# Kernel optimization log

Measured on AMD Instinct MI355X. Metric: run time of the kernel, lower is better.

Reference implementation:

```python
import jax, jax.numpy as jnp
import numpy as np

B, L, D, H = 2, 2048, 2048, 16
HD = D // H          # head_dim = 128
LAT = HD // 4        # latent_dim = 32


def setup_inputs() -> dict:
    key = jax.random.key(0)
    ks = jax.random.split(key, 16)
    def w(k, shape, fan_in):
        return jax.random.normal(k, shape, jnp.float32) / np.float32(np.sqrt(fan_in))
    x = jax.random.normal(ks[0], (B, L, D), jnp.float32)
    # RoPE frequencies, stored as (cos, sin) pairs: [L, HD//2, 2]
    inv_freq = 1.0 / (10000.0 ** (np.arange(0, HD, 2, dtype=np.float32) / HD))
    ang = np.outer(np.arange(L, dtype=np.float32), inv_freq)
    freqs_cis = jnp.stack([jnp.asarray(np.cos(ang)), jnp.asarray(np.sin(ang))], axis=-1)
    return dict(
        x=x, freqs_cis=freqs_cis,
        Wq=w(ks[1], (D, D), D), bq=jnp.zeros((D,), jnp.float32),
        Wk=w(ks[2], (D, D), D), bk=jnp.zeros((D,), jnp.float32),
        Wv=w(ks[3], (D, D), D), bv=jnp.zeros((D,), jnp.float32),
        Wqc=w(ks[4], (LAT, HD), HD), bqc=jnp.zeros((LAT,), jnp.float32),
        Wkc=w(ks[5], (LAT, HD), HD), bkc=jnp.zeros((LAT,), jnp.float32),
        Wvc=w(ks[6], (LAT, HD), HD), bvc=jnp.zeros((LAT,), jnp.float32),
        Wd=w(ks[7], (HD, LAT), LAT), bd=jnp.zeros((HD,), jnp.float32),
        Wo=w(ks[8], (D, D), D), bo=jnp.zeros((D,), jnp.float32),
    )


def _rope(t, freqs_cis):
    # t: [B,H,L,HD]; freqs_cis: [L, HD//2, 2] (cos, sin)
    tp = t.reshape(t.shape[:-1] + (HD // 2, 2))
    a, b = tp[..., 0], tp[..., 1]
    cr = freqs_cis[:, :, 0]  # [L, HD//2]
    ci = freqs_cis[:, :, 1]
    ra = a * cr - b * ci
    rb = a * ci + b * cr
    return jnp.stack([ra, rb], axis=-1).reshape(t.shape)


def reference(x, freqs_cis, Wq, bq, Wk, bk, Wv, bv, Wqc, bqc, Wkc, bkc, Wvc, bvc, Wd, bd, Wo, bo):
    Bx, Lx, Dx = x.shape
    # QKV projections -> [B,H,L,HD]
    def proj(W, bias):
        return (x @ W.T + bias).reshape(Bx, Lx, H, HD).transpose(0, 2, 1, 3)
    q = proj(Wq, bq)
    k = proj(Wk, bk)
    v = proj(Wv, bv)
    q = _rope(q, freqs_cis)
    k = _rope(k, freqs_cis)
    # per-head compression to latent dim: [B,H,L,LAT]
    qc = q @ Wqc.T + bqc
    kc = k @ Wkc.T + bkc
    vc = v @ Wvc.T + bvc
    scores = jnp.einsum('bhie,bhje->bhij', qc, kc) / np.float32(np.sqrt(LAT))
    mask = jnp.triu(jnp.ones((Lx, Lx), bool), 1)  # future positions
    scores = jnp.where(mask, jnp.float32(-jnp.inf), scores)
    probs = jax.nn.softmax(scores, axis=-1)
    attn = jnp.einsum('bhij,bhje->bhie', probs, vc)  # [B,H,L,LAT]
    attn = attn @ Wd.T + bd                          # decompress -> [B,H,L,HD]
    attn = attn.transpose(0, 2, 1, 3).reshape(Bx, Lx, Dx)
    return attn @ Wo.T + bo
```

## Files before the change

### kernel.cpp

```cpp
#include <hip/hip_runtime.h>

typedef __attribute__((ext_vector_type(8))) __bf16 bf16x8;
typedef __attribute__((ext_vector_type(4))) __bf16 bf16x4;
typedef __attribute__((ext_vector_type(4))) float f32x4;
typedef __attribute__((ext_vector_type(16))) float f32x16;

#define LL 2048
#define DD 2048
#define HH 16
#define HDIM 128

__global__ __launch_bounds__(256)
void setup_all(const float* __restrict__ x, const float* __restrict__ Wq,
               const float* __restrict__ Wk, const float* __restrict__ Wqc,
               const float* __restrict__ Wkc,
               const float* __restrict__ Wv, const float* __restrict__ Wvc,
               const float* __restrict__ bv, const float* __restrict__ bvc,
               const float* __restrict__ Wo, const float* __restrict__ Wd,
               const float* __restrict__ bd, const float* __restrict__ bo,
               __bf16* __restrict__ xb, __bf16* __restrict__ Wqb, __bf16* __restrict__ Wkb,
               __bf16* __restrict__ Wqcb, __bf16* __restrict__ Wkcb,
               __bf16* __restrict__ Wveff, float* __restrict__ bveff,
               __bf16* __restrict__ Woeff, float* __restrict__ boeff)
{
    __shared__ float sm[128 * 32];
    const int tid = threadIdx.x;
    const int bid = blockIdx.x;

    if (bid < 16392) {
        size_t i = (size_t)bid * 256 + tid;
        const float* s; __bf16* d; size_t off;
        if (i < 2097152)      { s = x;   d = xb;   off = i; }
        else if (i < 3145728) { s = Wq;  d = Wqb;  off = i - 2097152; }
        else if (i < 4194304) { s = Wk;  d = Wkb;  off = i - 3145728; }
        else if (i < 4195328) { s = Wqc; d = Wqcb; off = i - 4194304; }
        else                  { s = Wkc; d = Wkcb; off = i - 4195328; }
        float4 v = *(const float4*)(s + off * 4);
        bf16x4 o = { (__bf16)v.x, (__bf16)v.y, (__bf16)v.z, (__bf16)v.w };
        *(bf16x4*)(d + off * 4) = o;
        return;
    }
    int idx = bid - 16392;
    if (idx < 512) {
        float (*WvcT)[32] = (float(*)[32])sm;
        const int h = idx >> 5, dc = idx & 31;
        for (int i = tid; i < 4096; i += 256) WvcT[i & 127][i >> 7] = Wvc[i];
        __syncthreads();
        const int d  = dc * 64 + (tid & 63);
        const int o0 = (tid >> 6) * 8;
        float acc[8] = {};
        for (int jj = 0; jj < 128; ++jj) {
            const float w = Wv[(size_t)(h * 128 + jj) * 2048 + d];
            #pragma unroll
            for (int o = 0; o < 8; ++o) acc[o] += WvcT[jj][o0 + o] * w;
        }
        #pragma unroll
        for (int o = 0; o < 8; ++o)
            Wveff[(size_t)(h * 32 + o0 + o) * 2048 + d] = (__bf16)acc[o];
        if (dc == 0 && tid < 32) {
            float s = bvc[tid];
            for (int jj = 0; jj < 128; ++jj) s += WvcT[jj][tid] * bv[h * 128 + jj];
            bveff[h * 32 + tid] = s;
        }
        return;
    }
    idx -= 512;
    if (idx < 512) {
        float (*WdL)[32] = (float(*)[32])sm;
        const int dc = idx & 31, h = idx >> 5;
        for (int i = tid; i < 4096; i += 256) WdL[i >> 5][i & 31] = Wd[i];
        __syncthreads();
        const int dout = dc * 64 + (tid & 63);
        const int o0   = (tid >> 6) * 8;
        float acc[8] = {};
        const float* wrow = Wo + (size_t)dout * 2048 + h * 128;
        for (int u = 0; u < 128; ++u) {
            const float w = wrow[u];
            #pragma unroll
            for (int o = 0; o < 8; ++o) acc[o] += WdL[u][o0 + o] * w;
        }
        #pragma unroll
        for (int o = 0; o < 8; ++o)
            Woeff[(size_t)dout * 512 + h * 32 + o0 + o] = (__bf16)acc[o];
        return;
    }
    idx -= 512;
    float* bdL = sm;
    if (tid < 128) bdL[tid] = bd[tid];
    __syncthreads();
    const int d  = idx * 32 + (tid >> 3);
    const int s0 = (tid & 7) * 64;
    float s = 0.f;
    const float* wrow = Wo + (size_t)d * 2048 + s0 * 4;
    for (int c4 = 0; c4 < 64; ++c4) {
        float4 wv = *(const float4*)(wrow + c4 * 4);
        const int cb = ((s0 + c4) * 4) & 127;
        s += wv.x * bdL[cb] + wv.y * bdL[cb + 1] + wv.z * bdL[cb + 2] + wv.w * bdL[cb + 3];
    }
    #pragma unroll
    for (int off = 4; off; off >>= 1) s += __shfl_down(s, off, 8);
    if ((tid & 7) == 0) boeff[d] = bo[d] + s;
}

typedef unsigned int u32;
typedef const __attribute__((address_space(1))) u32* gp_t;
typedef __attribute__((address_space(3))) u32* lp_t;
__device__ __forceinline__ void gload16(const __bf16* g, __bf16* l)
{
    __builtin_amdgcn_global_load_lds((gp_t)(const void*)g, (lp_t)(void*)l, 16, 0, 0);
}

#define MF16(a, b, c) __builtin_amdgcn_mfma_f32_16x16x32_bf16(a, b, c, 0, 0, 0)

__global__ __launch_bounds__(256, 2)
void gemm_qkv(const __bf16* __restrict__ A,
              const __bf16* __restrict__ Wq, const __bf16* __restrict__ Wk,
              const __bf16* __restrict__ Wveff,
              const float* __restrict__ bq, const float* __restrict__ bk,
              const float* __restrict__ bveff,
              const __bf16* __restrict__ Wqcb, const __bf16* __restrict__ Wkcb,
              const float* __restrict__ bqc, const float* __restrict__ bkc,
              const float* __restrict__ fc,
              __bf16* __restrict__ qc, __bf16* __restrict__ kc, __bf16* __restrict__ vt)
{
    __shared__ __bf16 lds[3][12288];

    const int bid = blockIdx.x;
    const int xcd = bid & 7;
    const int j   = bid >> 3;
    const int bx  = j >> 2;
    const int byl = j & 3;
    const int by  = xcd * 4 + byl;
    const int m0  = by * 128;
    const int which = (bx >= 16) ? 2 : (bx >> 3);
    const int n0  = (which == 2) ? (bx - 16) * 256 : (bx & 7) * 256;
    const __bf16* W = which == 0 ? Wq : which == 1 ? Wk : Wveff;

    const int tid  = threadIdx.x;
    const int wid  = tid >> 6;
    const int lane = tid & 63;
    const int wr   = wid >> 1;
    const int wc   = wid & 1;
    const int l15  = lane & 15;
    const int l4   = lane >> 4;
    const int swz  = (l4 ^ (l15 & 3) ^ ((l15 >> 2) & 3)) * 8;

    const int srl  = lane >> 2;
    const int scol = ((lane & 3) ^ (srl & 3) ^ ((srl >> 2) & 3)) * 8;
    const __bf16* gA0 = A + (size_t)(m0 + wid * 32 + srl) * 2048 + scol;
    const __bf16* gB0 = W + (size_t)(n0 + wid * 64 + srl) * 2048 + scol;

    #define STAGE(bb, kk)                                                \
    {   __bf16* dA = &lds[bb][wid * 1024];                               \
        __bf16* dB = &lds[bb][4096 + wid * 2048];                        \
        gload16(gA0 + (kk), dA);                                         \
        gload16(gA0 + (size_t)16 * 2048 + (kk), dA + 512);               \
        gload16(gB0 + (kk), dB);                                         \
        gload16(gB0 + (size_t)16 * 2048 + (kk), dB + 512);               \
        gload16(gB0 + (size_t)32 * 2048 + (kk), dB + 1024);              \
        gload16(gB0 + (size_t)48 * 2048 + (kk), dB + 1536);              \
    }
    #define RD_A(bb, mf) (*(const bf16x8*)&lds[bb][(wr * 64 + (mf) * 16 + l15) * 32 + swz])
    #define RD_B(bb, nf) (*(const bf16x8*)&lds[bb][4096 + (wc * 128 + (nf) * 16 + l15) * 32 + swz])

    f32x4 acc[4][8] = {};

    STAGE(0, 0) STAGE(1, 32)
    asm volatile("s_waitcnt vmcnt(6)" ::: "memory");
    __builtin_amdgcn_s_barrier();

    #define TB(RB, SB, VM, DOST, kk)                                          \
    {                                                                         \
        bf16x8 fa[4], fb[8];                                                  \
        fa[0] = RD_A(RB, 0); fa[1] = RD_A(RB, 1);                             \
        fa[2] = RD_A(RB, 2); fa[3] = RD_A(RB, 3);                             \
        fb[0] = RD_B(RB, 0); fb[1] = RD_B(RB, 1);                             \
        fb[2] = RD_B(RB, 2); fb[3] = RD_B(RB, 3);                             \
        fb[4] = RD_B(RB, 4); fb[5] = RD_B(RB, 5);                             \
        fb[6] = RD_B(RB, 6); fb[7] = RD_B(RB, 7);                             \
        if (DOST) STAGE(SB, kk)                                               \
        asm volatile("s_waitcnt lgkmcnt(0)" ::: "memory");                    \
        __builtin_amdgcn_sched_barrier(0);                                    \
        __builtin_amdgcn_s_setprio(1);                                        \
        _Pragma("unroll")                                                     \
        for (int mf = 0; mf < 4; ++mf)                                        \
            _Pragma("unroll")                                                 \
            for (int nf = 0; nf < 8; ++nf)                                    \
                acc[mf][nf] = MF16(fa[mf], fb[nf], acc[mf][nf]);              \
        __builtin_amdgcn_s_setprio(0);                                        \
        asm volatile("s_waitcnt vmcnt(" VM ")" ::: "memory");                 \
        __builtin_amdgcn_s_barrier();                                         \
    }

    for (int tt = 0; tt < 60; tt += 3) {
        const int kk = (tt + 2) * 32;
        TB(0, 2, "6", true, kk)
        TB(1, 0, "6", true, kk + 32)
        TB(2, 1, "6", true, kk + 64)
    }
    TB(0, 2, "6", true, 62 * 32)
    TB(1, 0, "6", true, 63 * 32)
    TB(2, 0, "0", false, 0)
    TB(0, 0, "0", false, 0)
    #undef TB
    #undef STAGE
    #undef RD_A
    #undef RD_B

    if (which < 2) {
        __bf16* qt = &lds[0][0];
        const float* bb_ = which ? bk : bq;
        const __bf16* Wb = which ? Wkcb : Wqcb;
        const float*  bs = which ? bkc : bqc;
        const int o   = lane & 31;
        const int hi  = lane >> 5;
        const int b   = m0 >> 11;
        const int l0b = m0 & 2047;
        const int lrow = wid * 32 + o;
        const int l    = l0b + lrow;
        const float* fcr = fc + (size_t)l * 128;
        const float QSCALE = 0.17677669529663689f * 1.44269504088896340f;
        __bf16* outp = which ? kc : qc;

        bf16x8 wf[8];
        #pragma unroll
        for (int ks = 0; ks < 8; ++ks)
            wf[ks] = *(const bf16x8*)(Wb + o * 128 + ks * 16 + hi * 8);

        #pragma unroll
        for (int half = 0; half < 2; ++half) {
            if (wc == half) {
                #pragma unroll
                for (int nf = 0; nf < 8; ++nf) {
                    const int col = nf * 16 + l15;
                    const float bv = bb_[n0 + half * 128 + col];
                    #pragma unroll
                    for (int mf = 0; mf < 4; ++mf) {
                        const int row0 = wr * 64 + mf * 16 + l4 * 4;
                        #pragma unroll
                        for (int rr = 0; rr < 4; ++rr)
                            qt[(row0 + rr) * 136 + col] = (__bf16)(acc[mf][nf][rr] + bv);
                    }
                }
            }
            __syncthreads();

            const int h = (n0 >> 7) + half;
            f32x16 C = {};
            #pragma unroll
            for (int ks = 0; ks < 8; ++ks) {
                bf16x8 af = *(const bf16x8*)&qt[lrow * 136 + ks * 16 + hi * 8];
                const float4 cA = *(const float4*)(fcr + (ks * 8 + hi * 4) * 2);
                const float4 cB = *(const float4*)(fcr + (ks * 8 + hi * 4) * 2 + 4);
                float a, b_;
                a = (float)af[0]; b_ = (float)af[1];
                af[0] = (__bf16)(a * cA.x - b_ * cA.y); af[1] = (__bf16)(a * cA.y + b_ * cA.x);
                a = (float)af[2]; b_ = (float)af[3];
                af[2] = (__bf16)(a * cA.z - b_ * cA.w); af[3] = (__bf16)(a * cA.w + b_ * cA.z);
                a = (float)af[4]; b_ = (float)af[5];
                af[4] = (__bf16)(a * cB.x - b_ * cB.y); af[5] = (__bf16)(a * cB.y + b_ * cB.x);
                a = (float)af[6]; b_ = (float)af[7];
                af[6] = (__bf16)(a * cB.z - b_ * cB.w); af[7] = (__bf16)(a * cB.w + b_ * cB.z);
                C = __builtin_amdgcn_mfma_f32_32x32x16_bf16(af, wf[ks], C, 0, 0, 0);
            }

            const float bias = bs[o];
            const size_t g0row = (size_t)(b * 16 + h) * 2048 + l0b + wid * 32;
            #pragma unroll
            for (int r = 0; r < 16; ++r) {
                const int ro = (r & 3) + 8 * (r >> 2) + 4 * hi;
                float v = C[r] + bias;
                if (which == 0) v *= QSCALE;
                outp[(g0row + ro) * 32 + o] = (__bf16)v;
            }
            __syncthreads();
        }
    } else {
        #pragma unroll
        for (int nf = 0; nf < 8; ++nf) {
            const int ncol = n0 + wc * 128 + nf * 16 + l15;
            const float bv = bveff[ncol];
            const int hh = ncol >> 5, oo = ncol & 31;
            #pragma unroll
            for (int mf = 0; mf < 4; ++mf) {
                const int row0 = m0 + wr * 64 + mf * 16 + l4 * 4;
                const int b = row0 >> 11, l0 = row0 & 2047;
                bf16x4 pk = { (__bf16)(acc[mf][nf][0] + bv), (__bf16)(acc[mf][nf][1] + bv),
                              (__bf16)(acc[mf][nf][2] + bv), (__bf16)(acc[mf][nf][3] + bv) };
                *(bf16x4*)(vt + ((size_t)((b * 16 + hh) * 32 + oo)) * 2048 + l0) = pk;
            }
        }
    }
}

__global__ __launch_bounds__(256, 3)
void gemm_ao(const __bf16* __restrict__ ao, const __bf16* __restrict__ Woeff,
             const float* __restrict__ boeff, float* __restrict__ out)
{
    __shared__ __bf16 lds[3][2][4096];
    const int bid = blockIdx.x;
    const int xcd = bid & 7;
    const int jj  = bid >> 3;
    const int by  = xcd * 4 + (jj & 3);
    const int bx  = jj >> 2;
    const int m0  = by * 128;
    const int n0  = bx * 128;

    const int tid  = threadIdx.x;
    const int wid  = tid >> 6;
    const int lane = tid & 63;
    const int wr   = wid >> 1;
    const int wc   = wid & 1;
    const int l15  = lane & 15;
    const int l4   = lane >> 4;
    const int swz  = (l4 ^ (l15 & 3) ^ ((l15 >> 2) & 3)) * 8;

    const int srl  = lane >> 2;
    const int scol = ((lane & 3) ^ (srl & 3) ^ ((srl >> 2) & 3)) * 8;
    const int r0   = m0 + wid * 32 + srl;
    const int b0   = r0 >> 11, li0 = r0 & 2047;
    const __bf16* gA0 = ao + ((size_t)(b0 << 4) * 2048 + li0) * 32 + scol;
    const __bf16* gA1 = ao + ((size_t)(b0 << 4) * 2048 + li0 + 16) * 32 + scol;
    const __bf16* gB0 = Woeff + (size_t)(n0 + wid * 32 + srl) * 512 + scol;

    #define STAGE(bb, kk)                                                     \
    {   __bf16* dA = &lds[bb][0][wid * 1024];                                 \
        __bf16* dB = &lds[bb][1][wid * 1024];                                 \
        const size_t ka = (size_t)((kk) >> 5) * 65536;                        \
        gload16(gA0 + ka, dA);                                                \
        gload16(gA1 + ka, dA + 512);                                          \
        gload16(gB0 + (kk), dB);                                              \
        gload16(gB0 + (size_t)16 * 512 + (kk), dB + 512);                     \
    }
    #define RD_A(bb, mf) (*(const bf16x8*)&lds[bb][0][(wr * 64 + (mf) * 16 + l15) * 32 + swz])
    #define RD_B(bb, nf) (*(const bf16x8*)&lds[bb][1][(wc * 64 + (nf) * 16 + l15) * 32 + swz])

    f32x4 acc[4][4] = {};

    STAGE(0, 0) STAGE(1, 32)
    asm volatile("s_waitcnt vmcnt(4)" ::: "memory");
    __builtin_amdgcn_s_barrier();

    #define TB(RB, SB, VM, DOST, kk)                                          \
    {                                                                         \
        bf16x8 fa[4], fb[4];                                                  \
        fa[0] = RD_A(RB, 0); fa[1] = RD_A(RB, 1);                             \
        fa[2] = RD_A(RB, 2); fa[3] = RD_A(RB, 3);                             \
        fb[0] = RD_B(RB, 0); fb[1] = RD_B(RB, 1);                             \
        fb[2] = RD_B(RB, 2); fb[3] = RD_B(RB, 3);                             \
        if (DOST) STAGE(SB, kk)                                               \
        asm volatile("s_waitcnt lgkmcnt(0)" ::: "memory");                    \
        __builtin_amdgcn_sched_barrier(0);                                    \
        __builtin_amdgcn_s_setprio(1);                                        \
        _Pragma("unroll")                                                     \
        for (int mf = 0; mf < 4; ++mf)                                        \
            _Pragma("unroll")                                                 \
            for (int nf = 0; nf < 4; ++nf)                                    \
                acc[mf][nf] = MF16(fa[mf], fb[nf], acc[mf][nf]);              \
        __builtin_amdgcn_s_setprio(0);                                        \
        asm volatile("s_waitcnt vmcnt(" VM ")" ::: "memory");                 \
        __builtin_amdgcn_s_barrier();                                         \
    }

    for (int tt = 0; tt < 12; tt += 3) {
        const int kk = (tt + 2) * 32;
        TB(0, 2, "4", true, kk)
        TB(1, 0, "4", true, kk + 32)
        TB(2, 1, "4", true, kk + 64)
    }
    TB(0, 2, "4", true, 14 * 32)
    TB(1, 0, "4", true, 15 * 32)
    TB(2, 0, "0", false, 0)
    TB(0, 0, "0", false, 0)
    #undef TB
    #undef STAGE
    #undef RD_A
    #undef RD_B

    #pragma unroll
    for (int nf = 0; nf < 4; ++nf) {
        const int col = n0 + wc * 64 + nf * 16 + l15;
        const float bv = boeff[col];
        #pragma unroll
        for (int mf = 0; mf < 4; ++mf) {
            const int row0 = m0 + wr * 64 + mf * 16 + l4 * 4;
            #pragma unroll
            for (int rr = 0; rr < 4; ++rr)
                out[(size_t)(row0 + rr) * 2048 + col] = acc[mf][nf][rr] + bv;
        }
    }
}

__device__ __forceinline__ unsigned pkbf2(float a, float b)
{
    union { __bf16 h[2]; unsigned u; } x;
    x.h[0] = (__bf16)a; x.h[1] = (__bf16)b;
    return x.u;
}

#if __has_builtin(__builtin_amdgcn_permlane32_swap)
typedef unsigned int uint2v __attribute__((ext_vector_type(2)));
__device__ __forceinline__ void plswap(unsigned a, unsigned b, unsigned& w_lo, unsigned& w_hi, int)
{
    uint2v r = __builtin_amdgcn_permlane32_swap(a, b, false, false);
    w_lo = r[0]; w_hi = r[1];
}
#else
__device__ __forceinline__ void plswap(unsigned a, unsigned b, unsigned& w_lo, unsigned& w_hi, int hi)
{
    unsigned ax = (unsigned)__shfl_xor((int)a, 32);
    unsigned bx = (unsigned)__shfl_xor((int)b, 32);
    w_lo = hi ? bx : a;
    w_hi = hi ? b  : ax;
}
#endif

__global__ __launch_bounds__(256)
void attn_part(const __bf16* __restrict__ qc, const __bf16* __restrict__ kc,
               const __bf16* __restrict__ vt,
               float* __restrict__ pl, __bf16* __restrict__ po)
{
    const int bh  = blockIdx.x & 31;
    const int t_  = blockIdx.x >> 5;
    const int lin = t_ * 4 + (threadIdx.x >> 6);
    int g = (int)((sqrtf((float)lin + 1.0f) - 1.0f) * 0.5f);
    while (4 * (g + 1) * (g + 2) <= lin) ++g;
    while (4 * g * (g + 1) > lin) --g;
    const int rem = lin - 4 * g * (g + 1);
    const int sq  = rem / (g + 1);
    const int s   = 8 * g + sq;
    const int ci  = rem - sq * (g + 1);

    const int lane = threadIdx.x & 63;
    const int qcol = lane & 31;
    const int hi   = lane >> 5;

    const __bf16* qbase = qc + ((size_t)bh * LL + (size_t)s * 32) * 32;
    const __bf16* kbase = kc + (size_t)bh * LL * 32;
    const __bf16* vbase = vt + (size_t)bh * 32 * LL;

    const bf16x8 qf0 = *(const bf16x8*)(qbase + qcol * 32 + hi * 8);
    const bf16x8 qf1 = *(const bf16x8*)(qbase + qcol * 32 + 16 + hi * 8);

    const float M2 = 16.0f;
    float lsum = 0.f;
    f32x16 O = {};

    const int t0 = ci * 8;
    const int t1 = min(s, t0 + 7);

    const __bf16* krow = kbase + (size_t)(t0 * 32 + qcol) * 32 + hi * 8;
    const __bf16* vrow = vbase + (size_t)qcol * LL + t0 * 32 + hi * 8;
    bf16x8 kc0 = *(const bf16x8*)(krow);
    bf16x8 kc1 = *(const bf16x8*)(krow + 16);
    bf16x8 vc0 = *(const bf16x8*)(vrow);
    bf16x8 vc1 = *(const bf16x8*)(vrow + 16);

    for (int t = t0; t <= t1; ++t) {
        const int tn = (t < t1) ? t + 1 : t;
        const __bf16* krn = kbase + (size_t)(tn * 32 + qcol) * 32 + hi * 8;
        const __bf16* vrn = vbase + (size_t)qcol * LL + tn * 32 + hi * 8;
        bf16x8 kn0 = *(const bf16x8*)(krn);
        bf16x8 kn1 = *(const bf16x8*)(krn + 16);
        bf16x8 vn0 = *(const bf16x8*)(vrn);
        bf16x8 vn1 = *(const bf16x8*)(vrn + 16);

        f32x16 S = {};
        S = __builtin_amdgcn_mfma_f32_32x32x16_bf16(kc0, qf0, S, 0, 0, 0);
        S = __builtin_amdgcn_mfma_f32_32x32x16_bf16(kc1, qf1, S, 0, 0, 0);

        if (t == s) {
            #pragma unroll
            for (int r = 0; r < 16; ++r) {
                const int kl = (r & 3) + 8 * (r >> 2) + 4 * hi;
                if (kl > qcol) S[r] = -1e30f;
            }
        }
        float p[16];
        #pragma unroll
        for (int r = 0; r < 16; ++r) { p[r] = exp2f(S[r] - M2); lsum += p[r]; }

        unsigned w[8];
        #pragma unroll
        for (int i = 0; i < 8; ++i) w[i] = pkbf2(p[2 * i], p[2 * i + 1]);
        union PF { unsigned u[4]; bf16x8 v; } pf1, pf2;
        plswap(w[0], w[2], pf1.u[0], pf1.u[2], hi);
        plswap(w[1], w[3], pf1.u[1], pf1.u[3], hi);
        plswap(w[4], w[6], pf2.u[0], pf2.u[2], hi);
        plswap(w[5], w[7], pf2.u[1], pf2.u[3], hi);

        O = __builtin_amdgcn_mfma_f32_32x32x16_bf16(vc0, pf1.v, O, 0, 0, 0);
        O = __builtin_amdgcn_mfma_f32_32x32x16_bf16(vc1, pf2.v, O, 0, 0, 0);

        kc0 = kn0; kc1 = kn1; vc0 = vn0; vc1 = vn1;
    }

    const float L = lsum + __shfl_xor(lsum, 32);
    const size_t gq = (size_t)bh * LL + (size_t)s * 32 + qcol;
    const size_t slot = gq * 8 + ci;
    if (hi == 0) pl[slot] = L;
    __bf16* pp = po + slot * 32;
    #pragma unroll
    for (int g4 = 0; g4 < 4; ++g4) {
        bf16x4 pk = { (__bf16)O[g4 * 4 + 0], (__bf16)O[g4 * 4 + 1],
                      (__bf16)O[g4 * 4 + 2], (__bf16)O[g4 * 4 + 3] };
        *(bf16x4*)(pp + g4 * 8 + 4 * hi) = pk;
    }
}

__global__ __launch_bounds__(256)
void attn_comb(const float* __restrict__ pl, const __bf16* __restrict__ po,
               __bf16* __restrict__ ao)
{
    const int g = blockIdx.x * 256 + threadIdx.x;
    const int i = g & (LL - 1);
    const int nch = (i >> 8) + 1;
    float L = 0.f;
    float o[32] = {};
    for (int c = 0; c < nch; ++c) {
        L += pl[(size_t)g * 8 + c];
        const __bf16* pp = po + ((size_t)g * 8 + c) * 32;
        #pragma unroll
        for (int d8 = 0; d8 < 4; ++d8) {
            bf16x8 v = *(const bf16x8*)(pp + d8 * 8);
            #pragma unroll
            for (int jj = 0; jj < 8; ++jj) o[d8 * 8 + jj] += (float)v[jj];
        }
    }
    const float inv = 1.f / L;
    #pragma unroll
    for (int d8 = 0; d8 < 4; ++d8) {
        bf16x8 v;
        #pragma unroll
        for (int jj = 0; jj < 8; ++jj) v[jj] = (__bf16)(o[d8 * 8 + jj] * inv);
        *(bf16x8*)(ao + (size_t)g * 32 + d8 * 8) = v;
    }
}

extern "C" void kernel_launch(void* const* d_in, const int* in_sizes, int n_in,
                              void* d_out, int out_size, void* d_ws, size_t ws_size,
                              hipStream_t stream)
{
    const float* x   = (const float*)d_in[0];
    const float* fc  = (const float*)d_in[1];
    const float* Wq  = (const float*)d_in[2];
    const float* bq  = (const float*)d_in[3];
    const float* Wk  = (const float*)d_in[4];
    const float* bk  = (const float*)d_in[5];
    const float* Wv  = (const float*)d_in[6];
    const float* bv  = (const float*)d_in[7];
    const float* Wqc = (const float*)d_in[8];
    const float* bqc = (const float*)d_in[9];
    const float* Wkc = (const float*)d_in[10];
    const float* bkc = (const float*)d_in[11];
    const float* Wvc = (const float*)d_in[12];
    const float* bvc = (const float*)d_in[13];
    const float* Wd  = (const float*)d_in[14];
    const float* bd  = (const float*)d_in[15];
    const float* Wo  = (const float*)d_in[16];
    const float* bo  = (const float*)d_in[17];
    float* out = (float*)d_out;

    const size_t MB = 1048576;
    char* w = (char*)d_ws;
    __bf16* xb    = (__bf16*)(w);
    __bf16* Wqb   = (__bf16*)(w + 16 * MB);
    __bf16* Wkb   = (__bf16*)(w + 24 * MB);
    __bf16* Wveff = (__bf16*)(w + 32 * MB);
    __bf16* qcbf  = (__bf16*)(w + 66 * MB);
    __bf16* kcbf  = (__bf16*)(w + 70 * MB);
    __bf16* vtbf  = (__bf16*)(w + 74 * MB);
    __bf16* aobf  = (__bf16*)(w + 78 * MB);
    __bf16* Wqcb  = (__bf16*)(w + 82 * MB);
    __bf16* Wkcb  = (__bf16*)(w + 82 * MB + 8192);
    __bf16* Woeff = (__bf16*)(w + 83 * MB);
    float*  boeff = (float*)(w + 85 * MB);
    float*  bveff = (float*)(w + 85 * MB + 8192);

    __bf16* po = (__bf16*)d_ws;
    float*  pl = (float*)(w + 32 * MB);

    if (ws_size < (size_t)90 * MB) return;

    setup_all<<<17480, 256, 0, stream>>>(x, Wq, Wk, Wqc, Wkc, Wv, Wvc, bv, bvc,
                                         Wo, Wd, bd, bo,
                                         xb, Wqb, Wkb, Wqcb, Wkcb,
                                         Wveff, bveff, Woeff, boeff);

    gemm_qkv<<<576, 256, 0, stream>>>(xb, Wqb, Wkb, Wveff, bq, bk, bveff,
                                      Wqcb, Wkcb, bqc, bkc, fc, qcbf, kcbf, vtbf);

    attn_part<<<2304, 256, 0, stream>>>(qcbf, kcbf, vtbf, pl, po);
    attn_comb<<<256, 256, 0, stream>>>(pl, po, aobf);

    gemm_ao<<<512, 256, 0, stream>>>(aobf, Woeff, boeff, out);
}
```

Baseline: 215.4 us.

## Fuse split-K attention combine into partial kernel via atomic last-arriver reduction

Removes the separate attn_comb launch. Each attention wave bumps a per-(head, query-tile) counter after writing its partial, and the last-arriving wave sums all partials, normalizes and writes the output row. The counters are zeroed by an extra block in the setup kernel. This saves a kernel launch and a pass over the partials, at the cost of threadfences, atomics and an uneven tail of work on the last wave for each tile.

```diff
diff --git a/kernel.cpp b/kernel.cpp
--- a/kernel.cpp
+++ b/kernel.cpp
@@ -21,7 +21,8 @@
                __bf16* __restrict__ xb, __bf16* __restrict__ Wqb, __bf16* __restrict__ Wkb,
                __bf16* __restrict__ Wqcb, __bf16* __restrict__ Wkcb,
                __bf16* __restrict__ Wveff, float* __restrict__ bveff,
-               __bf16* __restrict__ Woeff, float* __restrict__ boeff)
+               __bf16* __restrict__ Woeff, float* __restrict__ boeff,
+               int* __restrict__ cnt)
 {
     __shared__ float sm[128 * 32];
     const int tid = threadIdx.x;
@@ -85,21 +86,25 @@
         return;
     }
     idx -= 512;
-    float* bdL = sm;
-    if (tid < 128) bdL[tid] = bd[tid];
-    __syncthreads();
-    const int d  = idx * 32 + (tid >> 3);
-    const int s0 = (tid & 7) * 64;
-    float s = 0.f;
-    const float* wrow = Wo + (size_t)d * 2048 + s0 * 4;
-    for (int c4 = 0; c4 < 64; ++c4) {
-        float4 wv = *(const float4*)(wrow + c4 * 4);
-        const int cb = ((s0 + c4) * 4) & 127;
-        s += wv.x * bdL[cb] + wv.y * bdL[cb + 1] + wv.z * bdL[cb + 2] + wv.w * bdL[cb + 3];
-    }
-    #pragma unroll
-    for (int off = 4; off; off >>= 1) s += __shfl_down(s, off, 8);
-    if ((tid & 7) == 0) boeff[d] = bo[d] + s;
+    if (idx < 64) {
+        float* bdL = sm;
+        if (tid < 128) bdL[tid] = bd[tid];
+        __syncthreads();
+        const int d  = idx * 32 + (tid >> 3);
+        const int s0 = (tid & 7) * 64;
+        float s = 0.f;
+        const float* wrow = Wo + (size_t)d * 2048 + s0 * 4;
+        for (int c4 = 0; c4 < 64; ++c4) {
+            float4 wv = *(const float4*)(wrow + c4 * 4);
+            const int cb = ((s0 + c4) * 4) & 127;
+            s += wv.x * bdL[cb] + wv.y * bdL[cb + 1] + wv.z * bdL[cb + 2] + wv.w * bdL[cb + 3];
+        }
+        #pragma unroll
+        for (int off = 4; off; off >>= 1) s += __shfl_down(s, off, 8);
+        if ((tid & 7) == 0) boeff[d] = bo[d] + s;
+        return;
+    }
+    for (int i = tid; i < 2048; i += 256) cnt[i] = 0;
 }
 
 typedef unsigned int u32;
@@ -418,7 +423,8 @@
 __global__ __launch_bounds__(256)
 void attn_part(const __bf16* __restrict__ qc, const __bf16* __restrict__ kc,
                const __bf16* __restrict__ vt,
-               float* __restrict__ pl, __bf16* __restrict__ po)
+               float* __restrict__ pl, __bf16* __restrict__ po,
+               int* __restrict__ cnt, __bf16* __restrict__ ao)
 {
     const int bh  = blockIdx.x & 31;
     const int t_  = blockIdx.x >> 5;
@@ -506,34 +512,38 @@
                       (__bf16)O[g4 * 4 + 2], (__bf16)O[g4 * 4 + 3] };
         *(bf16x4*)(pp + g4 * 8 + 4 * hi) = pk;
     }
-}
-
-__global__ __launch_bounds__(256)
-void attn_comb(const float* __restrict__ pl, const __bf16* __restrict__ po,
-               __bf16* __restrict__ ao)
-{
-    const int g = blockIdx.x * 256 + threadIdx.x;
-    const int i = g & (LL - 1);
-    const int nch = (i >> 8) + 1;
-    float L = 0.f;
-    float o[32] = {};
-    for (int c = 0; c < nch; ++c) {
-        L += pl[(size_t)g * 8 + c];
-        const __bf16* pp = po + ((size_t)g * 8 + c) * 32;
-        #pragma unroll
-        for (int d8 = 0; d8 < 4; ++d8) {
-            bf16x8 v = *(const bf16x8*)(pp + d8 * 8);
-            #pragma unroll
-            for (int jj = 0; jj < 8; ++jj) o[d8 * 8 + jj] += (float)v[jj];
-        }
-    }
-    const float inv = 1.f / L;
-    #pragma unroll
-    for (int d8 = 0; d8 < 4; ++d8) {
-        bf16x8 v;
-        #pragma unroll
-        for (int jj = 0; jj < 8; ++jj) v[jj] = (__bf16)(o[d8 * 8 + jj] * inv);
-        *(bf16x8*)(ao + (size_t)g * 32 + d8 * 8) = v;
+
+    const int nch = (s >> 3) + 1;
+    __threadfence();
+    int old = 0;
+    if (lane == 0) old = atomicAdd(&cnt[bh * 64 + s], 1);
+    old = __builtin_amdgcn_readfirstlane(old);
+    if (old == nch - 1) {
+        __threadfence();
+        const int q = lane & 31;
+        const size_t gq2 = (size_t)bh * LL + (size_t)s * 32 + q;
+        float Lt = 0.f;
+        float ov[16] = {};
+        for (int c = 0; c < nch; ++c) {
+            Lt += pl[gq2 * 8 + c];
+            const __bf16* p2 = po + (gq2 * 8 + c) * 32 + hi * 16;
+            bf16x8 v0 = *(const bf16x8*)(p2);
+            bf16x8 v1 = *(const bf16x8*)(p2 + 8);
+            #pragma unroll
+            for (int jj = 0; jj < 8; ++jj) {
+                ov[jj]     += (float)v0[jj];
+                ov[8 + jj] += (float)v1[jj];
+            }
+        }
+        const float inv = 1.f / Lt;
+        __bf16* aor = ao + gq2 * 32 + hi * 16;
+        #pragma unroll
+        for (int d8 = 0; d8 < 2; ++d8) {
+            bf16x8 vv;
+            #pragma unroll
+            for (int jj = 0; jj < 8; ++jj) vv[jj] = (__bf16)(ov[d8 * 8 + jj] * inv);
+            *(bf16x8*)(aor + d8 * 8) = vv;
+        }
     }
 }
 
@@ -577,21 +587,21 @@
     float*  boeff = (float*)(w + 85 * MB);
     float*  bveff = (float*)(w + 85 * MB + 8192);
 
-    __bf16* po = (__bf16*)d_ws;
-    float*  pl = (float*)(w + 32 * MB);
+    __bf16* po  = (__bf16*)d_ws;
+    float*  pl  = (float*)(w + 32 * MB);
+    int*    cnt = (int*)(w + 35 * MB);
 
     if (ws_size < (size_t)90 * MB) return;
 
-    setup_all<<<17480, 256, 0, stream>>>(x, Wq, Wk, Wqc, Wkc, Wv, Wvc, bv, bvc,
+    setup_all<<<17481, 256, 0, stream>>>(x, Wq, Wk, Wqc, Wkc, Wv, Wvc, bv, bvc,
                                          Wo, Wd, bd, bo,
                                          xb, Wqb, Wkb, Wqcb, Wkcb,
-                                         Wveff, bveff, Woeff, boeff);
+                                         Wveff, bveff, Woeff, boeff, cnt);
 
     gemm_qkv<<<576, 256, 0, stream>>>(xb, Wqb, Wkb, Wveff, bq, bk, bveff,
                                       Wqcb, Wkcb, bqc, bkc, fc, qcbf, kcbf, vtbf);
 
-    attn_part<<<2304, 256, 0, stream>>>(qcbf, kcbf, vtbf, pl, po);
-    attn_comb<<<256, 256, 0, stream>>>(pl, po, aobf);
+    attn_part<<<2304, 256, 0, stream>>>(qcbf, kcbf, vtbf, pl, po, cnt, aobf);
 
     gemm_ao<<<512, 256, 0, stream>>>(aobf, Woeff, boeff, out);
 }
```

After: 618.0 us. 187% more time.
